# Kernel optimization log

Measured on AMD Instinct MI355X. Metric: run time of the kernel, lower is better.

## Reference

```python
import jax, jax.numpy as jnp
import numpy as np


def _layer_norm(x, w, b, eps=1e-5):
    mu = jnp.mean(x, axis=-1, keepdims=True)
    var = jnp.mean((x - mu) ** 2, axis=-1, keepdims=True)
    return (x - mu) / jnp.sqrt(var + eps) * w + b


def _s4_block(u, log_dt, A_re, A_im, C_re, C_im, D, out_w, out_b):
    # u: (B, L, H). S4D diagonal SSM, bidirectional, ZOH discretization.
    B, L, H = u.shape
    dt = jnp.exp(log_dt)                       # (H,)
    A = A_re + 1j * A_im                       # (H, N) complex64
    dtA = A * dt[:, None]                      # (H, N)
    C = C_re + 1j * C_im                       # (2, H, N)
    Ct = C * ((jnp.exp(dtA) - 1.0) / A)        # (2, H, N)  ZOH input matrix folded into C
    vand = jnp.exp(dtA[:, :, None] * jnp.arange(L))   # (H, N, L) vandermonde of exp(dt*A)
    K = 2.0 * jnp.einsum('chn,hnl->chl', Ct, vand).real  # (2, H, L); 2*Re for conj pairs
    # bidirectional kernel laid out over length 2L (forward causal + flipped anticausal)
    k = jnp.pad(K[0], ((0, 0), (0, L))) + jnp.pad(jnp.flip(K[1], -1), ((0, 0), (L, 0)))
    k_f = jnp.fft.rfft(k, n=2 * L, axis=-1)    # (H, L+1)
    u_f = jnp.fft.rfft(u, n=2 * L, axis=1)     # (B, L+1, H)
    y = jnp.fft.irfft(u_f * k_f.T[None], n=2 * L, axis=1)[:, :L]  # (B, L, H)
    y = y + u * D                              # skip connection D*u
    y = jax.nn.gelu(y, approximate=False)      # torch GELU is exact erf form
    z = y @ out_w.T + out_b                    # (B, L, 2H) output linear
    return z[..., :H] * jax.nn.sigmoid(z[..., H:])  # GLU


def setup_inputs() -> dict:
    key = jax.random.key(0)
    ks = jax.random.split(key, 10)
    B, L, H, N, NL = 8, 4096, 512, 16, 4
    x = jax.random.normal(ks[0], (B, 1, L), dtype=jnp.float32)
    enc_w = jax.random.normal(ks[1], (H, 2), dtype=jnp.float32) * 0.1
    enc_b = jnp.zeros((H,), jnp.float32)
    # S4D-Lin init: dt log-uniform in [1e-3, 1e-1], A = -0.5 + i*pi*n
    log_dt = np.log(1e-3) + jax.random.uniform(ks[2], (NL, H), dtype=jnp.float32) * (np.log(1e-1) - np.log(1e-3))
    A_re = -0.5 * jnp.ones((NL, H, N), jnp.float32)
    A_im = jnp.broadcast_to(np.pi * jnp.arange(N, dtype=jnp.float32), (NL, H, N))
    C_re = jax.random.normal(ks[3], (NL, 2, H, N), dtype=jnp.float32) * 0.5
    C_im = jax.random.normal(ks[4], (NL, 2, H, N), dtype=jnp.float32) * 0.5
    D = jax.random.normal(ks[5], (NL, H), dtype=jnp.float32)
    out_w = jax.random.normal(ks[6], (NL, 2 * H, H), dtype=jnp.float32) / np.sqrt(H)
    out_b = jnp.zeros((NL, 2 * H), jnp.float32)
    ln_w = jnp.ones((NL, H), jnp.float32)
    ln_b = jnp.zeros((NL, H), jnp.float32)
    dec_w = jax.random.normal(ks[7], (1, H), dtype=jnp.float32) / np.sqrt(H)
    dec_b = jnp.zeros((1,), jnp.float32)
    return dict(x=x, enc_w=enc_w, enc_b=enc_b, log_dt=log_dt, A_re=A_re, A_im=A_im,
                C_re=C_re, C_im=C_im, D=D, out_w=out_w, out_b=out_b,
                ln_w=ln_w, ln_b=ln_b, dec_w=dec_w, dec_b=dec_b)


def reference(x, enc_w, enc_b, log_dt, A_re, A_im, C_re, C_im, D, out_w, out_b, ln_w, ln_b, dec_w, dec_b):
    B, _, L = x.shape
    grid = jnp.linspace(0.0, 1.0, L, dtype=x.dtype)                    # get_grid with grid=None
    h = jnp.concatenate([x.transpose(0, 2, 1),
                         jnp.broadcast_to(grid[None, :, None], (B, L, 1))], axis=-1)  # (B, L, 2)
    h = h @ enc_w.T + enc_b                                            # encoder -> (B, L, H)
    n_layers = log_dt.shape[0]
    for i in range(n_layers):                                          # prenorm residual stack
        z = _layer_norm(h, ln_w[i], ln_b[i])
        z = _s4_block(z, log_dt[i], A_re[i], A_im[i], C_re[i], C_im[i], D[i], out_w[i], out_b[i])
        h = z + h                                                      # dropout is identity (eval)
    y = h @ dec_w.T + dec_b                                            # decoder -> (B, L, 1)
    return y.transpose(0, 2, 1)                                        # (B, 1, L)
```

## Files before the change

### kernel.cpp

```cpp
#include <hip/hip_runtime.h>


typedef __attribute__((ext_vector_type(8))) short s16x8;
typedef __attribute__((ext_vector_type(4))) float f32x4;
typedef unsigned short u16;
typedef unsigned int u32;

#define LSEQ 4096
#define HD   512
#define NST  16
#define NLAYER 4
#define BS   8
#define LC   64
#define NCH  64
#define BC   512

static __device__ __forceinline__ u16 f2bf(float f){
  u32 u = __builtin_bit_cast(u32, f);
  u += 0x7FFFu + ((u >> 16) & 1u);
  return (u16)(u >> 16);
}
static __device__ __forceinline__ float bf2f(u16 v){
  u32 u = ((u32)v) << 16;
  return __builtin_bit_cast(float, u);
}
static __device__ __forceinline__ u32 pack2bf(float a, float b){
  return (u32)f2bf(a) | ((u32)f2bf(b) << 16);
}
static __device__ __forceinline__ float gelu_exact(float x){
  float z = fabsf(x) * 0.70710678118654752f;
  float t = 1.f / (1.f + 0.3275911f * z);
  float p = t*(0.254829592f + t*(-0.284496736f + t*(1.421413741f +
            t*(-1.453152027f + t*1.061405429f))));
  float er = 1.f - p * expf(-z*z);
  er = (x < 0.f) ? -er : er;
  return 0.5f * x * (1.f + er);
}

__global__ __launch_bounds__(256) void param_kernel(
    const float* __restrict__ log_dt, const float* __restrict__ A_re,
    const float* __restrict__ A_im, const float* __restrict__ C_re,
    const float* __restrict__ C_im, float* __restrict__ params)
{
  int idx = blockIdx.x*256 + threadIdx.x;
  int h = idx & (HD-1);
  int n = (idx >> 9) & (NST-1);
  int layer = idx >> 13;
  float dt  = expf(log_dt[layer*HD + h]);
  float Are = A_re[((layer<<9)+h)*NST + n];
  float Aim = A_im[((layer<<9)+h)*NST + n];
  float ar = Are*dt, ai = Aim*dt;
  float er = expf(ar), sn, cs;
  sincosf(ai, &sn, &cs);
  float wr = er*cs, wi = er*sn;
  float eL = expf((float)LC*ar), snL, csL;
  sincosf((float)LC*ai, &snL, &csL);
  float* P = params + layer*65536;
  P[n*1024 + h]        = wr;
  P[n*1024 + 512 + h]  = wi;
  P[16384 + n*1024 + h]       = eL*csL;
  P[16384 + n*1024 + 512 + h] = eL*snL;
  float den = Are*Are + Aim*Aim;
  float qr = ((wr-1.f)*Are + wi*Aim) / den;
  float qi = (wi*Are - (wr-1.f)*Aim) / den;
  #pragma unroll
  for (int d=0; d<2; d++){
    float Cre = C_re[(((layer*2+d)<<9)+h)*NST + n];
    float Cim = C_im[(((layer*2+d)<<9)+h)*NST + n];
    P[32768 + (d*NST+n)*1024 + h]       = 2.f*(Cre*qr - Cim*qi);
    P[32768 + (d*NST+n)*1024 + 512 + h] = 2.f*(Cre*qi + Cim*qr);
  }
}

__global__ __launch_bounds__(256) void owconv_kernel(const float* __restrict__ ow,
                                                     u16* __restrict__ owbf)
{
  size_t idx = (size_t)blockIdx.x*256 + threadIdx.x;
  owbf[idx] = f2bf(ow[idx]);
}

__global__ __launch_bounds__(256) void encoder_kernel(
    const float* __restrict__ x, const float* __restrict__ ew,
    const float* __restrict__ eb, float* __restrict__ hbuf,
    float2* __restrict__ pstat)
{
  int row  = (int)((blockIdx.x*256 + threadIdx.x) >> 6);
  int lane = threadIdx.x & 63;
  int t = row & (LSEQ-1);
  int b = row >> 12;
  float xv = x[(b<<12) + t];
  float g = (float)t * (1.0f/4095.0f);
  const float* ewp = ew + lane*16;
  const float* ebp = eb + lane*8;
  float hv[8], s = 0.f, sq = 0.f;
  #pragma unroll
  for (int j=0;j<8;++j){
    float v = xv*ewp[2*j] + g*ewp[2*j+1] + ebp[j];
    hv[j] = v; s += v; sq += v*v;
  }
  float4* hp = (float4*)(hbuf + ((size_t)row << 9) + lane*8);
  hp[0] = make_float4(hv[0],hv[1],hv[2],hv[3]);
  hp[1] = make_float4(hv[4],hv[5],hv[6],hv[7]);
  #pragma unroll
  for (int off=32; off; off>>=1){ s += __shfl_xor(s, off, 64); sq += __shfl_xor(sq, off, 64); }
  if (lane < 8) pstat[(size_t)row*8 + lane] = (lane==0) ? make_float2(s, sq)
                                                        : make_float2(0.f, 0.f);
}

__global__ __launch_bounds__(256) void lnt_kernel(
    const float* __restrict__ hbuf, const float2* __restrict__ pstat,
    const float* __restrict__ lnw, const float* __restrict__ lnb,
    u16* __restrict__ uT)
{
  __shared__ u32 tile[512*33];
  __shared__ float smu[64], srs[64];
  int bc = blockIdx.x, tid = threadIdx.x;
  const float* base = hbuf + ((size_t)bc << 15);
  if (tid < 64){
    const float2* pp = pstat + ((size_t)(bc*64 + tid))*8;
    float s = 0.f, sq = 0.f;
    #pragma unroll
    for (int j=0;j<8;++j){ float2 v = pp[j]; s += v.x; sq += v.y; }
    float mu = s*(1.f/512.f);
    float var = sq*(1.f/512.f) - mu*mu;
    smu[tid] = mu; srs[tid] = rsqrtf(var + 1e-5f);
  }
  __syncthreads();
  #pragma unroll
  for (int it=0; it<8; ++it){
    int ho = (tid & 7) + it*8;
    int tp = (tid >> 3) & 31;
    int r0 = 2*tp, r1 = 2*tp + 1;
    float mu0 = smu[r0], rs0 = srs[r0];
    float mu1 = smu[r1], rs1 = srs[r1];
    const float* pa = base + ((size_t)r0 << 9) + ho*8;
    const float* pc = base + ((size_t)r1 << 9) + ho*8;
    float4 a0 = *(const float4*)pa, a1 = *(const float4*)(pa+4);
    float4 c0 = *(const float4*)pc, c1 = *(const float4*)(pc+4);
    const float* pw = lnw + ho*8;
    const float* pb = lnb + ho*8;
    float4 w0 = *(const float4*)pw, w1 = *(const float4*)(pw+4);
    float4 b0 = *(const float4*)pb, b1 = *(const float4*)(pb+4);
    u32* td = &tile[(ho*8)*33 + tp];
    td[0*33] = pack2bf((a0.x-mu0)*rs0*w0.x+b0.x, (c0.x-mu1)*rs1*w0.x+b0.x);
    td[1*33] = pack2bf((a0.y-mu0)*rs0*w0.y+b0.y, (c0.y-mu1)*rs1*w0.y+b0.y);
    td[2*33] = pack2bf((a0.z-mu0)*rs0*w0.z+b0.z, (c0.z-mu1)*rs1*w0.z+b0.z);
    td[3*33] = pack2bf((a0.w-mu0)*rs0*w0.w+b0.w, (c0.w-mu1)*rs1*w0.w+b0.w);
    td[4*33] = pack2bf((a1.x-mu0)*rs0*w1.x+b1.x, (c1.x-mu1)*rs1*w1.x+b1.x);
    td[5*33] = pack2bf((a1.y-mu0)*rs0*w1.y+b1.y, (c1.y-mu1)*rs1*w1.y+b1.y);
    td[6*33] = pack2bf((a1.z-mu0)*rs0*w1.z+b1.z, (c1.z-mu1)*rs1*w1.z+b1.z);
    td[7*33] = pack2bf((a1.w-mu0)*rs0*w1.w+b1.w, (c1.w-mu1)*rs1*w1.w+b1.w);
  }
  __syncthreads();
  #pragma unroll
  for (int it=0; it<16; ++it){
    int linear = it*256 + tid;
    int h = linear >> 3, sg = linear & 7;
    uint4 v = *(const uint4*)&tile[h*33 + sg*4];
    *(uint4*)(uT + ((size_t)h*BC + bc)*64 + sg*8) = v;
  }
}

__global__ __launch_bounds__(256) void build_kernel(
    const float* __restrict__ logdt, const float* __restrict__ Are_,
    const float* __restrict__ Aim_, const float* __restrict__ P,
    const float* __restrict__ Dv, u16* __restrict__ Abuf, u16* __restrict__ Wbuf)
{
  __shared__ float pr[65][17], pi[65][17];
  __shared__ float kp0[4][64], kp1[4][64];
  __shared__ float kk0[64], kk1[64];
  int h = blockIdx.x;
  int tid = threadIdx.x;
  int d = tid & 63, ng = tid >> 6;
  float dt = expf(logdt[h]);
  float k0p = 0.f, k1p = 0.f;
  #pragma unroll
  for (int j=0; j<4; ++j){
    int n = ng*4 + j;
    float ar = Are_[h*NST+n]*dt, ai = Aim_[h*NST+n]*dt;
    float er = expf(ar*(float)d), sn, cs;
    sincosf(ai*(float)d, &sn, &cs);
    float wr = er*cs, wi = er*sn;
    pr[d][n] = wr; pi[d][n] = wi;
    if (d == 63){
      float er2 = expf(ar*64.f), sn2, cs2;
      sincosf(ai*64.f, &sn2, &cs2);
      pr[64][n] = er2*cs2; pi[64][n] = er2*sn2;
    }
    float c0r = P[32768 + n*1024 + h],      c0i = P[32768 + n*1024 + 512 + h];
    float c1r = P[32768 + (16+n)*1024 + h], c1i = P[32768 + (16+n)*1024 + 512 + h];
    k0p += c0r*wr - c0i*wi;
    k1p += c1r*wr - c1i*wi;
  }
  kp0[ng][d] = k0p; kp1[ng][d] = k1p;
  __syncthreads();
  if (ng == 0){
    kk0[d] = kp0[0][d]+kp0[1][d]+kp0[2][d]+kp0[3][d];
    kk1[d] = kp1[0][d]+kp1[1][d]+kp1[2][d]+kp1[3][d];
  }
  __syncthreads();
  {
    int r = d;
    u32* wdst = (u32*)(Wbuf + (size_t)h*4096 + r*64);
    int n = r & 15;
    #pragma unroll
    for (int k=0;k<8;++k){
      int s2 = ng*8 + k;
      int s0 = 2*s2, s1 = s0+1;
      float va, vb;
      if      (r < 16){ va = pr[63-s0][n]; vb = pr[63-s1][n]; }
      else if (r < 32){ va = pi[63-s0][n]; vb = pi[63-s1][n]; }
      else if (r < 48){ va = pr[s0][n];    vb = pr[s1][n]; }
      else            { va = pi[s0][n];    vb = pi[s1][n]; }
      wdst[s2] = pack2bf(va, vb);
    }
  }
  {
    int t = d;
    float Dh = Dv[h];
    u32* adst = (u32*)(Abuf + (size_t)h*8192 + t*128);
    #pragma unroll
    for (int k=0;k<8;++k){
      int j2 = ng*8 + k;
      int j0 = 2*j2, j1 = j0+1;
      float va = (j0 < t) ? kk0[t-j0] : ((j0 == t) ? (kk0[0] + Dh) : kk1[j0-t-1]);
      float vb = (j1 < t) ? kk0[t-j1] : ((j1 == t) ? (kk0[0] + Dh) : kk1[j1-t-1]);
      adst[j2] = pack2bf(va, vb);
    }
    #pragma unroll
    for (int j=0;j<4;j+=2){
      int n = ng*4 + j;
      float ar0 = pr[t+1][n],   ai0 = pi[t+1][n];
      float ar1 = pr[t+1][n+1], ai1 = pi[t+1][n+1];
      float br0 = pr[63-t][n],   bi0 = pi[63-t][n];
      float br1 = pr[63-t][n+1], bi1 = pi[63-t][n+1];
      float c0r0 = P[32768 + n*1024 + h],     c0i0 = P[32768 + n*1024 + 512 + h];
      float c0r1 = P[32768 + (n+1)*1024 + h], c0i1 = P[32768 + (n+1)*1024 + 512 + h];
      float c1r0 = P[32768 + (16+n)*1024 + h], c1i0 = P[32768 + (16+n)*1024 + 512 + h];
      float c1r1 = P[32768 + (17+n)*1024 + h], c1i1 = P[32768 + (17+n)*1024 + 512 + h];
      int g = n >> 1;
      adst[32      + g] = pack2bf(c0r0*ar0 - c0i0*ai0,    c0r1*ar1 - c0i1*ai1);
      adst[32 + 8  + g] = pack2bf(-(c0r0*ai0 + c0i0*ar0), -(c0r1*ai1 + c0i1*ar1));
      adst[32 + 16 + g] = pack2bf(c1r0*br0 - c1i0*bi0,    c1r1*br1 - c1i1*bi1);
      adst[32 + 24 + g] = pack2bf(-(c1r0*bi0 + c1i0*br0), -(c1r1*bi1 + c1i1*br1));
    }
  }
}

__global__ __launch_bounds__(256) void g1_kernel(
    const u16* __restrict__ Wbuf, const u16* __restrict__ uT, u16* __restrict__ Sraw)
{
  int h = blockIdx.x >> 1, half = blockIdx.x & 1;
  int tid = threadIdx.x, wave = tid >> 6, lane = tid & 63;
  int ro = lane & 15, qq = lane >> 4;
  const u16* Wh = Wbuf + (size_t)h*4096;
  const u16* Uh = uT + (size_t)h*BC*64;
  f32x4 acc[4][4];
  #pragma unroll
  for (int i=0;i<4;i++)
    #pragma unroll
    for (int j=0;j<4;j++)
      #pragma unroll
      for (int k=0;k<4;k++) acc[i][j][k] = 0.f;
  #pragma unroll
  for (int ks=0; ks<2; ++ks){
    s16x8 a[4], b[4];
    #pragma unroll
    for (int mt=0; mt<4; ++mt){
      uint4 v = *(const uint4*)(Wh + (mt*16 + ro)*64 + ks*32 + qq*8);
      a[mt] = __builtin_bit_cast(s16x8, v);
    }
    #pragma unroll
    for (int nt=0; nt<4; ++nt){
      int bc = half*256 + wave*64 + nt*16 + ro;
      uint4 v = *(const uint4*)(Uh + (size_t)bc*64 + ks*32 + qq*8);
      b[nt] = __builtin_bit_cast(s16x8, v);
    }
    #pragma unroll
    for (int mt=0; mt<4; ++mt)
      #pragma unroll
      for (int nt=0; nt<4; ++nt)
        acc[mt][nt] = __builtin_amdgcn_mfma_f32_16x16x32_bf16(a[mt], b[nt], acc[mt][nt], 0, 0, 0);
  }
  #pragma unroll
  for (int mt=0; mt<4; ++mt)
    #pragma unroll
    for (int nt=0; nt<4; ++nt){
      int bc = half*256 + wave*64 + nt*16 + ro;
      int r0 = mt*16 + qq*4;
      u32 lo = pack2bf(acc[mt][nt][0], acc[mt][nt][1]);
      u32 hi = pack2bf(acc[mt][nt][2], acc[mt][nt][3]);
      *(uint2*)(Sraw + ((size_t)h*BC + bc)*64 + r0) = make_uint2(lo, hi);
    }
}

__global__ __launch_bounds__(256) void p2_kernel(
    const float* __restrict__ P, const u16* __restrict__ Sraw, u16* __restrict__ V)
{
  int gid = blockIdx.x*256 + threadIdx.x;
  int n   = gid & 15;
  int b   = (gid >> 4) & 7;
  int dir = (gid >> 7) & 1;
  int h   = gid >> 8;
  float wLr = P[16384 + n*1024 + h];
  float wLi = P[16384 + n*1024 + 512 + h];
  const u16* sp = Sraw + ((size_t)h*BC + b*64)*64;
  u16*       vp = V    + ((size_t)h*BC + b*64)*64;
  float Xr = 0.f, Xi = 0.f;
  if (dir == 0){
    for (int c=0; c<NCH; ++c){
      vp[c*64 + n]      = f2bf(Xr);
      vp[c*64 + 16 + n] = f2bf(Xi);
      float sr = bf2f(sp[c*64 + n]), si = bf2f(sp[c*64 + 16 + n]);
      float nr = fmaf(wLr, Xr, fmaf(-wLi, Xi, sr));
      float ni = fmaf(wLr, Xi, fmaf( wLi, Xr, si));
      Xr = nr; Xi = ni;
    }
  } else {
    for (int cc=0; cc<NCH; ++cc){
      int c = NCH-1-cc;
      vp[c*64 + 32 + n] = f2bf(Xr);
      vp[c*64 + 48 + n] = f2bf(Xi);
      float sr = bf2f(sp[c*64 + 32 + n]), si = bf2f(sp[c*64 + 48 + n]);
      float nr = fmaf(wLr, Xr, fmaf(-wLi, Xi, sr));
      float ni = fmaf(wLr, Xi, fmaf( wLi, Xr, si));
      Xr = nr; Xi = ni;
    }
  }
}

__global__ __launch_bounds__(256) void g2_kernel(
    const u16* __restrict__ Abuf, const u16* __restrict__ uT,
    const u16* __restrict__ V, u16* __restrict__ yT)
{
  int h = blockIdx.x >> 1, half = blockIdx.x & 1;
  int tid = threadIdx.x, wave = tid >> 6, lane = tid & 63;
  int ro = lane & 15, qq = lane >> 4;
  const u16* Ah = Abuf + (size_t)h*8192;
  const u16* Uh = uT + (size_t)h*BC*64;
  const u16* Vh = V  + (size_t)h*BC*64;
  f32x4 acc[4][4];
  #pragma unroll
  for (int i=0;i<4;i++)
    #pragma unroll
    for (int j=0;j<4;j++)
      #pragma unroll
      for (int k=0;k<4;k++) acc[i][j][k] = 0.f;
  #pragma unroll
  for (int ks=0; ks<4; ++ks){
    const u16* Bsrc = (ks < 2) ? Uh : Vh;
    int koff = (ks & 1)*32 + qq*8;
    s16x8 a[4], b[4];
    #pragma unroll
    for (int mt=0; mt<4; ++mt){
      uint4 v = *(const uint4*)(Ah + (mt*16 + ro)*128 + ks*32 + qq*8);
      a[mt] = __builtin_bit_cast(s16x8, v);
    }
    #pragma unroll
    for (int nt=0; nt<4; ++nt){
      int bc = half*256 + wave*64 + nt*16 + ro;
      uint4 v = *(const uint4*)(Bsrc + (size_t)bc*64 + koff);
      b[nt] = __builtin_bit_cast(s16x8, v);
    }
    #pragma unroll
    for (int mt=0; mt<4; ++mt)
      #pragma unroll
      for (int nt=0; nt<4; ++nt)
        acc[mt][nt] = __builtin_amdgcn_mfma_f32_16x16x32_bf16(a[mt], b[nt], acc[mt][nt], 0, 0, 0);
  }
  #pragma unroll
  for (int mt=0; mt<4; ++mt)
    #pragma unroll
    for (int nt=0; nt<4; ++nt){
      int bc = half*256 + wave*64 + nt*16 + ro;
      int t0 = mt*16 + qq*4;
      u32 lo = pack2bf(gelu_exact(acc[mt][nt][0]), gelu_exact(acc[mt][nt][1]));
      u32 hi = pack2bf(gelu_exact(acc[mt][nt][2]), gelu_exact(acc[mt][nt][3]));
      *(uint2*)(yT + ((size_t)h*BC + bc)*64 + t0) = make_uint2(lo, hi);
    }
}

__global__ __launch_bounds__(256) void t2_kernel(const u16* __restrict__ yT,
                                                 u16* __restrict__ uy)
{
  __shared__ u32 tile[64*257];
  int bc = blockIdx.x, tid = threadIdx.x;
  #pragma unroll
  for (int it=0; it<8; ++it){
    int sg = tid & 7;
    int hp = it*32 + (tid >> 3);
    const u16* s0 = yT + ((size_t)(2*hp)*BC + bc)*64 + sg*8;
    uint4 a = *(const uint4*)s0;
    uint4 b = *(const uint4*)(s0 + (size_t)BC*64);
    u32 ua[4] = {a.x,a.y,a.z,a.w}, ub[4] = {b.x,b.y,b.z,b.w};
    #pragma unroll
    for (int w=0; w<4; ++w){
      u32 lo = (ua[w] & 0xFFFFu) | (ub[w] << 16);
      u32 hi = (ua[w] >> 16) | (ub[w] & 0xFFFF0000u);
      tile[(sg*8 + 2*w    )*257 + hp] = lo;
      tile[(sg*8 + 2*w + 1)*257 + hp] = hi;
    }
  }
  __syncthreads();
  #pragma unroll
  for (int it=0; it<16; ++it){
    int linear = it*256 + tid;
    int t = linear >> 6, sg = linear & 63;
    uint4 v = *(const uint4*)&tile[t*257 + sg*4];
    *(uint4*)(uy + ((size_t)(bc*64 + t) << 9) + sg*8) = v;
  }
}

static __device__ __forceinline__ void async16(const void* g, void* l){
  __builtin_amdgcn_global_load_lds((const __attribute__((address_space(1))) unsigned*)g,
                                   (__attribute__((address_space(3))) unsigned*)l,
                                   16, 0, 0);
}
__global__ __launch_bounds__(256) void gemm_glu_kernel(
    const u16* __restrict__ ybf, const u16* __restrict__ owbf,
    const float* __restrict__ ob, float* __restrict__ hbuf,
    float2* __restrict__ pstat)
{
  __shared__ u16 As[128*64];
  __shared__ u16 Bsh[128*64];
  const int tid = threadIdx.x;
  const int wave = tid >> 6, lane = tid & 63;
  const int x7 = blockIdx.x & 7;
  const int nt = (blockIdx.x >> 3) & 7;
  const int mt = (blockIdx.x >> 6)*8 + x7;
  const int m0 = mt*128, n0 = nt*64;
  const int row = tid >> 3;
  const int ch  = tid & 7;
  f32x4 acc[2][8];
  #pragma unroll
  for (int i=0;i<2;i++)
    #pragma unroll
    for (int j=0;j<8;j++)
      #pragma unroll
      for (int k=0;k<4;k++) acc[i][j][k] = 0.f;

  const int ro = lane & 15, qq = lane >> 4;
  const int sx = ro & 7;
  for (int k0=0;k0<512;k0+=64){
    __syncthreads();
    #pragma unroll
    for (int p=0;p<4;p++){
      int r = p*32 + row;
      int cs = (ch ^ (r & 7)) << 3;
      async16(ybf + ((size_t)(m0+r) << 9) + k0 + cs, &As[(r<<6) + (ch<<3)]);
      int br = n0 + (r & 63) + ((r >> 6) << 9);
      async16(owbf + ((size_t)br << 9) + k0 + cs, &Bsh[(r<<6) + (ch<<3)]);
    }
    __syncthreads();
    #pragma unroll
    for (int ks=0;ks<2;ks++){
      s16x8 a[2], bf[8];
      #pragma unroll
      for (int mi=0;mi<2;mi++){
        int g = ks*4 + qq;
        uint4 t = *(const uint4*)(&As[((wave*32 + mi*16 + ro)<<6) + ((g ^ sx)<<3)]);
        a[mi] = __builtin_bit_cast(s16x8, t);
      }
      #pragma unroll
      for (int ni=0;ni<8;ni++){
        int g = ks*4 + qq;
        uint4 t = *(const uint4*)(&Bsh[((ni*16 + ro)<<6) + ((g ^ sx)<<3)]);
        bf[ni] = __builtin_bit_cast(s16x8, t);
      }
      #pragma unroll
      for (int mi=0;mi<2;mi++)
        #pragma unroll
        for (int ni=0;ni<8;ni++)
          acc[mi][ni] = __builtin_amdgcn_mfma_f32_16x16x32_bf16(a[mi], bf[ni], acc[mi][ni], 0, 0, 0);
    }
  }
  float b1v[4], b2v[4];
  #pragma unroll
  for (int ni=0;ni<4;ni++){ b1v[ni] = ob[n0 + ni*16 + ro]; b2v[ni] = ob[n0 + ni*16 + ro + 512]; }
  #pragma unroll
  for (int mi=0;mi<2;mi++){
    #pragma unroll
    for (int rg=0;rg<4;rg++){
      int rowi = m0 + wave*32 + mi*16 + qq*4 + rg;
      float s = 0.f, sq = 0.f;
      #pragma unroll
      for (int ni=0;ni<4;ni++){
        int col = n0 + ni*16 + ro;
        float zz1 = acc[mi][ni][rg] + b1v[ni];
        float zz2 = acc[mi][ni+4][rg] + b2v[ni];
        float g = zz1 / (1.f + expf(-zz2));
        size_t idx = ((size_t)rowi << 9) + col;
        float hn = hbuf[idx] + g;
        hbuf[idx] = hn;
        s += hn; sq += hn*hn;
      }
      #pragma unroll
      for (int off=1; off<16; off<<=1){ s += __shfl_xor(s, off, 64); sq += __shfl_xor(sq, off, 64); }
      if (ro == 0) pstat[(size_t)rowi*8 + nt] = make_float2(s, sq);
    }
  }
}

__global__ __launch_bounds__(256) void decoder_kernel(
    const float* __restrict__ hbuf, const float* __restrict__ dec_w,
    const float* __restrict__ dec_b, float* __restrict__ out)
{
  int wid  = (int)((blockIdx.x*256 + threadIdx.x) >> 6);
  int lane = threadIdx.x & 63;
  const float* p = hbuf + ((size_t)wid << 9) + lane*8;
  float4 a = *(const float4*)p;
  float4 b = *(const float4*)(p+4);
  const float* dw = dec_w + lane*8;
  float4 w0 = *(const float4*)dw;
  float4 w1 = *(const float4*)(dw+4);
  float s = a.x*w0.x + a.y*w0.y + a.z*w0.z + a.w*w0.w
          + b.x*w1.x + b.y*w1.y + b.z*w1.z + b.w*w1.w;
  #pragma unroll
  for (int off=32; off; off>>=1) s += __shfl_xor(s, off, 64);
  if (lane == 0) out[wid] = s + dec_b[0];
}

extern "C" void kernel_launch(void* const* d_in, const int* in_sizes, int n_in,
                              void* d_out, int out_size, void* d_ws, size_t ws_size,
                              hipStream_t stream) {
  const float* x     = (const float*)d_in[0];
  const float* encw  = (const float*)d_in[1];
  const float* encb  = (const float*)d_in[2];
  const float* logdt = (const float*)d_in[3];
  const float* A_re  = (const float*)d_in[4];
  const float* A_im  = (const float*)d_in[5];
  const float* C_re  = (const float*)d_in[6];
  const float* C_im  = (const float*)d_in[7];
  const float* Dv    = (const float*)d_in[8];
  const float* out_w = (const float*)d_in[9];
  const float* out_b = (const float*)d_in[10];
  const float* ln_w  = (const float*)d_in[11];
  const float* ln_b  = (const float*)d_in[12];
  const float* dec_w = (const float*)d_in[13];
  const float* dec_b = (const float*)d_in[14];

  char* ws = (char*)d_ws;
  float*  hbuf   = (float*) (ws);
  u16*    uy     = (u16*)   (ws + 67108864);
  u16*    uT     = (u16*)   (ws + 100663296);
  u16*    Sraw   = (u16*)   (ws + 134217728);
  u16*    Vbuf   = (u16*)   (ws + 167772160);
  u16*    owbf   = (u16*)   (ws + 201326592);
  float*  params = (float*) (ws + 205520896);
  u16*    Abuf   = (u16*)   (ws + 206569472);
  u16*    Wbuf   = (u16*)   (ws + 214958080);
  float2* pstat  = (float2*)(ws + 219152384);
  u16*    yT     = Sraw;

  param_kernel<<<128, 256, 0, stream>>>(logdt, A_re, A_im, C_re, C_im, params);
  owconv_kernel<<<8192, 256, 0, stream>>>(out_w, owbf);
  encoder_kernel<<<8192, 256, 0, stream>>>(x, encw, encb, hbuf, pstat);
  for (int layer=0; layer<NLAYER; ++layer){
    const float* P = params + layer*65536;
    lnt_kernel<<<512, 256, 0, stream>>>(hbuf, pstat, ln_w + layer*HD, ln_b + layer*HD, uT);
    build_kernel<<<512, 256, 0, stream>>>(logdt + layer*HD, A_re + layer*HD*NST,
                                          A_im + layer*HD*NST, P, Dv + layer*HD,
                                          Abuf, Wbuf);
    g1_kernel<<<1024, 256, 0, stream>>>(Wbuf, uT, Sraw);
    p2_kernel<<<512, 256, 0, stream>>>(P, Sraw, Vbuf);
    g2_kernel<<<1024, 256, 0, stream>>>(Abuf, uT, Vbuf, yT);
    t2_kernel<<<512, 256, 0, stream>>>(yT, uy);
    gemm_glu_kernel<<<2048, 256, 0, stream>>>(uy, owbf + (size_t)layer*524288,
                                              out_b + layer*1024, hbuf, pstat);
  }
  decoder_kernel<<<8192, 256, 0, stream>>>(hbuf, dec_w, dec_b, (float*)d_out);
}
```

Baseline: 829.9 us.

## Fuse chunk-state GEMM, inter-chunk scan and output GEMM into one LDS-resident SSM kernel

Replaces the three kernels g1 (chunk state projection), p2 (sequential scan over chunks) and g2 (output GEMM plus GELU) with one kernel per head. Each head's input tile is loaded into LDS with async loads and an XOR swizzle, and the scanned state is kept in LDS instead of round-tripping through global memory. This removes the Sraw and V global traffic and two launches per layer. In exchange, the grid drops from 1024 to 512 blocks, two 32KB LDS buffers limit occupancy, and the serial scan runs on only 128 threads while the rest of the block waits at a barrier.

```diff
diff --git a/kernel.cpp b/kernel.cpp
--- a/kernel.cpp
+++ b/kernel.cpp
@@ -35,6 +35,11 @@
   float er = 1.f - p * expf(-z*z);
   er = (x < 0.f) ? -er : er;
   return 0.5f * x * (1.f + er);
+}
+static __device__ __forceinline__ void async16(const void* g, void* l){
+  __builtin_amdgcn_global_load_lds((const __attribute__((address_space(1))) unsigned*)g,
+                                   (__attribute__((address_space(3))) unsigned*)l,
+                                   16, 0, 0);
 }
 
 __global__ __launch_bounds__(256) void param_kernel(
@@ -247,137 +252,151 @@
   }
 }
 
-__global__ __launch_bounds__(256) void g1_kernel(
-    const u16* __restrict__ Wbuf, const u16* __restrict__ uT, u16* __restrict__ Sraw)
-{
-  int h = blockIdx.x >> 1, half = blockIdx.x & 1;
-  int tid = threadIdx.x, wave = tid >> 6, lane = tid & 63;
-  int ro = lane & 15, qq = lane >> 4;
+__global__ __launch_bounds__(256) void ssm_kernel(
+    const float* __restrict__ P, const u16* __restrict__ Wbuf,
+    const u16* __restrict__ Abuf, const u16* __restrict__ uT,
+    u16* __restrict__ yT)
+{
+  __shared__ u16 Ul[256*64];
+  __shared__ u16 Vl[256*64];
+  const int h = blockIdx.x;
+  const int tid = threadIdx.x;
+  const int wave = tid >> 6, lane = tid & 63;
+  const int ro = lane & 15, qq = lane >> 4;
+  const int sx = ro & 7;
   const u16* Wh = Wbuf + (size_t)h*4096;
-  const u16* Uh = uT + (size_t)h*BC*64;
-  f32x4 acc[4][4];
-  #pragma unroll
-  for (int i=0;i<4;i++)
-    #pragma unroll
-    for (int j=0;j<4;j++)
-      #pragma unroll
-      for (int k=0;k<4;k++) acc[i][j][k] = 0.f;
-  #pragma unroll
-  for (int ks=0; ks<2; ++ks){
-    s16x8 a[4], b[4];
-    #pragma unroll
-    for (int mt=0; mt<4; ++mt){
-      uint4 v = *(const uint4*)(Wh + (mt*16 + ro)*64 + ks*32 + qq*8);
-      a[mt] = __builtin_bit_cast(s16x8, v);
-    }
-    #pragma unroll
-    for (int nt=0; nt<4; ++nt){
-      int bc = half*256 + wave*64 + nt*16 + ro;
-      uint4 v = *(const uint4*)(Uh + (size_t)bc*64 + ks*32 + qq*8);
-      b[nt] = __builtin_bit_cast(s16x8, v);
-    }
-    #pragma unroll
-    for (int mt=0; mt<4; ++mt)
-      #pragma unroll
-      for (int nt=0; nt<4; ++nt)
-        acc[mt][nt] = __builtin_amdgcn_mfma_f32_16x16x32_bf16(a[mt], b[nt], acc[mt][nt], 0, 0, 0);
-  }
-  #pragma unroll
-  for (int mt=0; mt<4; ++mt)
-    #pragma unroll
-    for (int nt=0; nt<4; ++nt){
-      int bc = half*256 + wave*64 + nt*16 + ro;
-      int r0 = mt*16 + qq*4;
-      u32 lo = pack2bf(acc[mt][nt][0], acc[mt][nt][1]);
-      u32 hi = pack2bf(acc[mt][nt][2], acc[mt][nt][3]);
-      *(uint2*)(Sraw + ((size_t)h*BC + bc)*64 + r0) = make_uint2(lo, hi);
-    }
-}
-
-__global__ __launch_bounds__(256) void p2_kernel(
-    const float* __restrict__ P, const u16* __restrict__ Sraw, u16* __restrict__ V)
-{
-  int gid = blockIdx.x*256 + threadIdx.x;
-  int n   = gid & 15;
-  int b   = (gid >> 4) & 7;
-  int dir = (gid >> 7) & 1;
-  int h   = gid >> 8;
-  float wLr = P[16384 + n*1024 + h];
-  float wLi = P[16384 + n*1024 + 512 + h];
-  const u16* sp = Sraw + ((size_t)h*BC + b*64)*64;
-  u16*       vp = V    + ((size_t)h*BC + b*64)*64;
-  float Xr = 0.f, Xi = 0.f;
-  if (dir == 0){
-    for (int c=0; c<NCH; ++c){
-      vp[c*64 + n]      = f2bf(Xr);
-      vp[c*64 + 16 + n] = f2bf(Xi);
-      float sr = bf2f(sp[c*64 + n]), si = bf2f(sp[c*64 + 16 + n]);
-      float nr = fmaf(wLr, Xr, fmaf(-wLi, Xi, sr));
-      float ni = fmaf(wLr, Xi, fmaf( wLi, Xr, si));
-      Xr = nr; Xi = ni;
-    }
-  } else {
-    for (int cc=0; cc<NCH; ++cc){
-      int c = NCH-1-cc;
-      vp[c*64 + 32 + n] = f2bf(Xr);
-      vp[c*64 + 48 + n] = f2bf(Xi);
-      float sr = bf2f(sp[c*64 + 32 + n]), si = bf2f(sp[c*64 + 48 + n]);
-      float nr = fmaf(wLr, Xr, fmaf(-wLi, Xi, sr));
-      float ni = fmaf(wLr, Xi, fmaf( wLi, Xr, si));
-      Xr = nr; Xi = ni;
-    }
-  }
-}
-
-__global__ __launch_bounds__(256) void g2_kernel(
-    const u16* __restrict__ Abuf, const u16* __restrict__ uT,
-    const u16* __restrict__ V, u16* __restrict__ yT)
-{
-  int h = blockIdx.x >> 1, half = blockIdx.x & 1;
-  int tid = threadIdx.x, wave = tid >> 6, lane = tid & 63;
-  int ro = lane & 15, qq = lane >> 4;
   const u16* Ah = Abuf + (size_t)h*8192;
   const u16* Uh = uT + (size_t)h*BC*64;
-  const u16* Vh = V  + (size_t)h*BC*64;
-  f32x4 acc[4][4];
-  #pragma unroll
-  for (int i=0;i<4;i++)
-    #pragma unroll
-    for (int j=0;j<4;j++)
-      #pragma unroll
-      for (int k=0;k<4;k++) acc[i][j][k] = 0.f;
-  #pragma unroll
-  for (int ks=0; ks<4; ++ks){
-    const u16* Bsrc = (ks < 2) ? Uh : Vh;
-    int koff = (ks & 1)*32 + qq*8;
-    s16x8 a[4], b[4];
-    #pragma unroll
-    for (int mt=0; mt<4; ++mt){
-      uint4 v = *(const uint4*)(Ah + (mt*16 + ro)*128 + ks*32 + qq*8);
-      a[mt] = __builtin_bit_cast(s16x8, v);
-    }
-    #pragma unroll
-    for (int nt=0; nt<4; ++nt){
-      int bc = half*256 + wave*64 + nt*16 + ro;
-      uint4 v = *(const uint4*)(Bsrc + (size_t)bc*64 + koff);
-      b[nt] = __builtin_bit_cast(s16x8, v);
-    }
-    #pragma unroll
-    for (int mt=0; mt<4; ++mt)
-      #pragma unroll
-      for (int nt=0; nt<4; ++nt)
-        acc[mt][nt] = __builtin_amdgcn_mfma_f32_16x16x32_bf16(a[mt], b[nt], acc[mt][nt], 0, 0, 0);
-  }
-  #pragma unroll
-  for (int mt=0; mt<4; ++mt)
-    #pragma unroll
-    for (int nt=0; nt<4; ++nt){
-      int bc = half*256 + wave*64 + nt*16 + ro;
-      int t0 = mt*16 + qq*4;
-      u32 lo = pack2bf(gelu_exact(acc[mt][nt][0]), gelu_exact(acc[mt][nt][1]));
-      u32 hi = pack2bf(gelu_exact(acc[mt][nt][2]), gelu_exact(acc[mt][nt][3]));
-      *(uint2*)(yT + ((size_t)h*BC + bc)*64 + t0) = make_uint2(lo, hi);
-    }
+
+  for (int half=0; half<2; ++half){
+    if (half) __syncthreads();
+    #pragma unroll
+    for (int i=0; i<8; ++i){
+      int r = i*32 + (tid >> 3);
+      int gch = tid & 7;
+      const u16* src = Uh + ((size_t)(half*256 + r))*64 + ((gch ^ (r & 7)) << 3);
+      async16(src, &Ul[i*2048 + tid*8]);
+    }
+    __syncthreads();
+    {
+      f32x4 acc[4][4];
+      #pragma unroll
+      for (int i=0;i<4;i++)
+        #pragma unroll
+        for (int j=0;j<4;j++)
+          #pragma unroll
+          for (int k=0;k<4;k++) acc[i][j][k] = 0.f;
+      #pragma unroll
+      for (int ks=0; ks<2; ++ks){
+        int g = ks*4 + qq;
+        s16x8 a[4], b[4];
+        #pragma unroll
+        for (int mt=0; mt<4; ++mt){
+          uint4 v = *(const uint4*)(Wh + (mt*16 + ro)*64 + ks*32 + qq*8);
+          a[mt] = __builtin_bit_cast(s16x8, v);
+        }
+        #pragma unroll
+        for (int nt=0; nt<4; ++nt){
+          int bl = wave*64 + nt*16 + ro;
+          uint4 v = *(const uint4*)(&Ul[bl*64 + ((g ^ sx) << 3)]);
+          b[nt] = __builtin_bit_cast(s16x8, v);
+        }
+        #pragma unroll
+        for (int mt=0; mt<4; ++mt)
+          #pragma unroll
+          for (int nt=0; nt<4; ++nt)
+            acc[mt][nt] = __builtin_amdgcn_mfma_f32_16x16x32_bf16(a[mt], b[nt], acc[mt][nt], 0, 0, 0);
+      }
+      #pragma unroll
+      for (int mt=0; mt<4; ++mt)
+        #pragma unroll
+        for (int nt=0; nt<4; ++nt){
+          int bl = wave*64 + nt*16 + ro;
+          int r0 = mt*16 + qq*4;
+          u32 lo = pack2bf(acc[mt][nt][0], acc[mt][nt][1]);
+          u32 hi = pack2bf(acc[mt][nt][2], acc[mt][nt][3]);
+          int addr = bl*64 + (((r0 >> 3) ^ (bl & 7)) << 3) + (r0 & 7);
+          *(uint2*)(&Vl[addr]) = make_uint2(lo, hi);
+        }
+    }
+    __syncthreads();
+    if (tid < 128){
+      int n   = tid & 15;
+      int bl4 = (tid >> 4) & 3;
+      int dir = (tid >> 6) & 1;
+      float wLr = P[16384 + n*1024 + h];
+      float wLi = P[16384 + n*1024 + 512 + h];
+      float Xr = 0.f, Xi = 0.f;
+      if (dir == 0){
+        int kA = n, kB = 16 + n;
+        for (int c=0; c<NCH; ++c){
+          int bl = bl4*64 + c;
+          int aA = bl*64 + (((kA >> 3) ^ (c & 7)) << 3) + (kA & 7);
+          int aB = bl*64 + (((kB >> 3) ^ (c & 7)) << 3) + (kB & 7);
+          float sr = bf2f(Vl[aA]), si = bf2f(Vl[aB]);
+          Vl[aA] = f2bf(Xr); Vl[aB] = f2bf(Xi);
+          float nr = fmaf(wLr, Xr, fmaf(-wLi, Xi, sr));
+          float ni = fmaf(wLr, Xi, fmaf( wLi, Xr, si));
+          Xr = nr; Xi = ni;
+        }
+      } else {
+        int kA = 32 + n, kB = 48 + n;
+        for (int cc=0; cc<NCH; ++cc){
+          int c = NCH-1-cc;
+          int bl = bl4*64 + c;
+          int aA = bl*64 + (((kA >> 3) ^ (c & 7)) << 3) + (kA & 7);
+          int aB = bl*64 + (((kB >> 3) ^ (c & 7)) << 3) + (kB & 7);
+          float sr = bf2f(Vl[aA]), si = bf2f(Vl[aB]);
+          Vl[aA] = f2bf(Xr); Vl[aB] = f2bf(Xi);
+          float nr = fmaf(wLr, Xr, fmaf(-wLi, Xi, sr));
+          float ni = fmaf(wLr, Xi, fmaf( wLi, Xr, si));
+          Xr = nr; Xi = ni;
+        }
+      }
+    }
+    __syncthreads();
+    {
+      f32x4 acc[4][4];
+      #pragma unroll
+      for (int i=0;i<4;i++)
+        #pragma unroll
+        for (int j=0;j<4;j++)
+          #pragma unroll
+          for (int k=0;k<4;k++) acc[i][j][k] = 0.f;
+      #pragma unroll
+      for (int ks=0; ks<4; ++ks){
+        const u16* Bsrc = (ks < 2) ? Ul : Vl;
+        int g = (ks & 1)*4 + qq;
+        s16x8 a[4], b[4];
+        #pragma unroll
+        for (int mt=0; mt<4; ++mt){
+          uint4 v = *(const uint4*)(Ah + (mt*16 + ro)*128 + ks*32 + qq*8);
+          a[mt] = __builtin_bit_cast(s16x8, v);
+        }
+        #pragma unroll
+        for (int nt=0; nt<4; ++nt){
+          int bl = wave*64 + nt*16 + ro;
+          uint4 v = *(const uint4*)(&Bsrc[bl*64 + ((g ^ sx) << 3)]);
+          b[nt] = __builtin_bit_cast(s16x8, v);
+        }
+        #pragma unroll
+        for (int mt=0; mt<4; ++mt)
+          #pragma unroll
+          for (int nt=0; nt<4; ++nt)
+            acc[mt][nt] = __builtin_amdgcn_mfma_f32_16x16x32_bf16(a[mt], b[nt], acc[mt][nt], 0, 0, 0);
+      }
+      #pragma unroll
+      for (int mt=0; mt<4; ++mt)
+        #pragma unroll
+        for (int nt=0; nt<4; ++nt){
+          int bc = half*256 + wave*64 + nt*16 + ro;
+          int t0 = mt*16 + qq*4;
+          u32 lo = pack2bf(gelu_exact(acc[mt][nt][0]), gelu_exact(acc[mt][nt][1]));
+          u32 hi = pack2bf(gelu_exact(acc[mt][nt][2]), gelu_exact(acc[mt][nt][3]));
+          *(uint2*)(yT + ((size_t)h*BC + bc)*64 + t0) = make_uint2(lo, hi);
+        }
+    }
+  }
 }
 
 __global__ __launch_bounds__(256) void t2_kernel(const u16* __restrict__ yT,
@@ -411,11 +430,6 @@
   }
 }
 
-static __device__ __forceinline__ void async16(const void* g, void* l){
-  __builtin_amdgcn_global_load_lds((const __attribute__((address_space(1))) unsigned*)g,
-                                   (__attribute__((address_space(3))) unsigned*)l,
-                                   16, 0, 0);
-}
 __global__ __launch_bounds__(256) void gemm_glu_kernel(
     const u16* __restrict__ ybf, const u16* __restrict__ owbf,
     const float* __restrict__ ob, float* __restrict__ hbuf,
@@ -543,14 +557,12 @@
   float*  hbuf   = (float*) (ws);
   u16*    uy     = (u16*)   (ws + 67108864);
   u16*    uT     = (u16*)   (ws + 100663296);
-  u16*    Sraw   = (u16*)   (ws + 134217728);
-  u16*    Vbuf   = (u16*)   (ws + 167772160);
+  u16*    yT     = (u16*)   (ws + 134217728);
   u16*    owbf   = (u16*)   (ws + 201326592);
   float*  params = (float*) (ws + 205520896);
   u16*    Abuf   = (u16*)   (ws + 206569472);
   u16*    Wbuf   = (u16*)   (ws + 214958080);
   float2* pstat  = (float2*)(ws + 219152384);
-  u16*    yT     = Sraw;
 
   param_kernel<<<128, 256, 0, stream>>>(logdt, A_re, A_im, C_re, C_im, params);
   owconv_kernel<<<8192, 256, 0, stream>>>(out_w, owbf);
@@ -561,9 +573,7 @@
     build_kernel<<<512, 256, 0, stream>>>(logdt + layer*HD, A_re + layer*HD*NST,
                                           A_im + layer*HD*NST, P, Dv + layer*HD,
                                           Abuf, Wbuf);
-    g1_kernel<<<1024, 256, 0, stream>>>(Wbuf, uT, Sraw);
-    p2_kernel<<<512, 256, 0, stream>>>(P, Sraw, Vbuf);
-    g2_kernel<<<1024, 256, 0, stream>>>(Abuf, uT, Vbuf, yT);
+    ssm_kernel<<<512, 256, 0, stream>>>(P, Wbuf, Abuf, uT, yT);
     t2_kernel<<<512, 256, 0, stream>>>(yT, uy);
     gemm_glu_kernel<<<2048, 256, 0, stream>>>(uy, owbf + (size_t)layer*524288,
                                               out_b + layer*1024, hbuf, pstat);
```

Result: faster. 764.1 us (-7.9%).
